# Kernel optimization log

Measured on AMD Instinct MI355X. Metric: run time of the kernel, lower is better.

Reference implementation:

```python
import jax, jax.numpy as jnp
import numpy as np
import math

B, T, C = 8, 2048, 1024
KEY_SIZE, VALUE_SIZE = 1024, 1024


def setup_inputs() -> dict:
    key = jax.random.key(0)
    ks = jax.random.split(key, 7)
    s = 1.0 / math.sqrt(C)
    return {
        "input": jax.random.normal(ks[0], (B, T, C), dtype=jnp.float32),
        "mask": jnp.ones((B, T, 1), dtype=jnp.float32),
        "Wq": jax.random.uniform(ks[1], (C, KEY_SIZE), jnp.float32, -s, s),
        "bq": jax.random.uniform(ks[2], (KEY_SIZE,), jnp.float32, -s, s),
        "Wk": jax.random.uniform(ks[3], (C, KEY_SIZE), jnp.float32, -s, s),
        "bk": jax.random.uniform(ks[4], (KEY_SIZE,), jnp.float32, -s, s),
        "Wv": jax.random.uniform(ks[5], (C, VALUE_SIZE), jnp.float32, -s, s),
        "bv": jax.random.uniform(ks[6], (VALUE_SIZE,), jnp.float32, -s, s),
    }


def reference(input, mask, Wq, bq, Wk, bk, Wv, bv):
    # QKV projections: [B, T, C] @ [C, K] -> [B, T, K]
    query = input @ Wq + bq
    keys = input @ Wk + bk
    values = input @ Wv + bv
    # scores[b, tq, tk] = query[b, tq, :] . keys[b, tk, :]
    scores = jnp.einsum("bqk,btk->bqt", query, keys) / math.sqrt(KEY_SIZE)
    # NOTE: softmax over the QUERY dimension (axis=1), as in the original (dim=1)
    attn = jax.nn.softmax(scores, axis=1)
    out = jnp.einsum("bqt,btv->bqv", attn, values)
    return out * mask
```

## Files before the change

kernel.cpp:

```cpp
#include <hip/hip_runtime.h>
#include <hip/hip_bf16.h>
#include <cstdint>

typedef __attribute__((ext_vector_type(8))) __bf16 bf16x8;
typedef __attribute__((ext_vector_type(4))) float f32x4;
typedef __attribute__((ext_vector_type(8))) unsigned short u16x8;

static __device__ __forceinline__ unsigned short f2b(float f) {
    union { float f; unsigned u; } v; v.f = f;
    unsigned r = v.u + 0x7fffu + ((v.u >> 16) & 1u);
    return (unsigned short)(r >> 16);
}
static __device__ __forceinline__ float b2f(unsigned short b) {
    union { unsigned u; float f; } v; v.u = ((unsigned)b) << 16;
    return v.f;
}

#define LL16(g, l) __builtin_amdgcn_global_load_lds( \
    (const __attribute__((address_space(1))) void*)(g), \
    (__attribute__((address_space(3))) void*)(l), 16, 0, 0)

#define BAR() __builtin_amdgcn_s_barrier()
#define WAIT_VM6() asm volatile("s_waitcnt vmcnt(6)" ::: "memory")
#define WAIT_VM0() asm volatile("s_waitcnt vmcnt(0)" ::: "memory")

__global__ void conv_f32_bf16(const float* __restrict__ in,
                              unsigned short* __restrict__ out, long n8) {
    long i = (long)blockIdx.x * blockDim.x + threadIdx.x;
    if (i >= n8) return;
    const float4* p = (const float4*)in + i * 2;
    float4 a = p[0], b = p[1];
    u16x8 r;
    r[0] = f2b(a.x); r[1] = f2b(a.y); r[2] = f2b(a.z); r[3] = f2b(a.w);
    r[4] = f2b(b.x); r[5] = f2b(b.y); r[6] = f2b(b.z); r[7] = f2b(b.w);
    *(u16x8*)(out + i * 8) = r;
}

__global__ void transpose_w(const float* __restrict__ w0,
                            const float* __restrict__ w1,
                            const float* __restrict__ w2,
                            unsigned short* __restrict__ out) {
    __shared__ float tile[32][33];
    int z = blockIdx.z;
    const float* W = (z == 0) ? w0 : (z == 1) ? w1 : w2;
    int n0 = blockIdx.x * 32, c0 = blockIdx.y * 32;
    int tx = threadIdx.x & 31, ty = threadIdx.x >> 5;
    #pragma unroll
    for (int i = 0; i < 32; i += 8)
        tile[ty + i][tx] = W[(long)(c0 + ty + i) * 1024 + n0 + tx];
    __syncthreads();
    unsigned short* o = out + (long)z * 1024 * 1024;
    #pragma unroll
    for (int i = 0; i < 32; i += 8)
        o[(long)(n0 + ty + i) * 1024 + c0 + tx] = f2b(tile[tx][ty + i]);
}

__global__ void scale_vt(unsigned short* __restrict__ Vt,
                         const float* __restrict__ colsum) {
    long i8 = ((long)blockIdx.x * 256 + threadIdx.x) * 8;
    int b = (int)(i8 >> 21);
    int rem = (int)(i8 & ((1 << 21) - 1));
    int t = rem & 2047;
    const float* cs = colsum + b * 2048 + t;
    u16x8 v = *(const u16x8*)(Vt + i8);
    u16x8 o;
    #pragma unroll
    for (int j = 0; j < 8; ++j) o[j] = f2b(b2f(v[j]) / cs[j]);
    *(u16x8*)(Vt + i8) = o;
}


#define RD_A(h) do { _Pragma("unroll") for (int mi = 2*(h); mi < 2*(h)+2; ++mi) { \
    af[mi][0] = *(const bf16x8*)(lds + aBase + baA + mi*1024 + cx0); \
    af[mi][1] = *(const bf16x8*)(lds + aBase + baA + mi*1024 + cx1); } } while (0)
#define RD_B(h) do { _Pragma("unroll") for (int nj = 2*(h); nj < 2*(h)+2; ++nj) { \
    bf[nj][0] = *(const bf16x8*)(lds + bBase + baB + nj*1024 + cx0); \
    bf[nj][1] = *(const bf16x8*)(lds + bBase + baB + nj*1024 + cx1); } } while (0)
#define MMA_Q(a, b) do { \
    __builtin_amdgcn_s_setprio(1); \
    _Pragma("unroll") for (int mi = 2*(a); mi < 2*(a)+2; ++mi) \
    _Pragma("unroll") for (int nj = 2*(b); nj < 2*(b)+2; ++nj) { \
        acc[mi][nj] = __builtin_amdgcn_mfma_f32_16x16x32_bf16( \
            af[mi][0], bf[nj][0], acc[mi][nj], 0, 0, 0); \
        acc[mi][nj] = __builtin_amdgcn_mfma_f32_16x16x32_bf16( \
            af[mi][1], bf[nj][1], acc[mi][nj], 0, 0, 0); } \
    __builtin_amdgcn_s_setprio(0); } while (0)

template<int MODE>
__global__ __launch_bounds__(512, 2)
void gemm256x128(const unsigned short* __restrict__ Aall,
                 const unsigned short* __restrict__ Ball,
                 void* __restrict__ Cv,
                 int M, int N, int K, int ldc,
                 long aStride, long bStride, long cStride,
                 const float* __restrict__ aux, float* __restrict__ colsum) {
    __shared__ unsigned short lds[73728];

    const int gx = gridDim.x, gy = gridDim.y;
    const int nxy = gx * gy;
    const int nwg = nxy * gridDim.z;
    const int orig = (blockIdx.z * gy + blockIdx.y) * gx + blockIdx.x;
    const int swz = (orig & 7) * (nwg >> 3) + (orig >> 3);
    const int bz = swz / nxy;
    const int rem = swz - bz * nxy;
    const int by = rem / gx;
    const int bx = rem - by * gx;

    const unsigned short* A  = Aall + (long)bz * aStride;
    const unsigned short* Bt = Ball + (long)bz * bStride;

    const int tid = threadIdx.x;
    const int lane = tid & 63;
    const int w = tid >> 6;
    const int wrow = w >> 1, wcol = w & 1;
    const int lr = lane & 15, lg = lane >> 4;

    const int bm = by * 256, bn = bx * 128;
    const int NT = K >> 6;

    const int r0 = tid >> 3;
    const int c0 = (tid & 7) ^ (r0 & 7);
    const unsigned short* sA0 = A  + (long)(bm + r0)       * K + c0 * 8;
    const unsigned short* sA1 = A  + (long)(bm + 64 + r0)  * K + c0 * 8;
    const unsigned short* sA2 = A  + (long)(bm + 128 + r0) * K + c0 * 8;
    const unsigned short* sA3 = A  + (long)(bm + 192 + r0) * K + c0 * 8;
    const unsigned short* sB0 = Bt + (long)(bn + r0)       * K + c0 * 8;
    const unsigned short* sB1 = Bt + (long)(bn + 64 + r0)  * K + c0 * 8;
    const int dstT = tid * 8;

    const int cx0 = (lg ^ (lr & 7)) * 8;
    const int cx1 = ((4 + lg) ^ (lr & 7)) * 8;
    const int baA = (wrow * 64 + lr) * 64;
    const int baB = (wcol * 64 + lr) * 64;

    bf16x8 af[4][2], bf[4][2];
    f32x4 acc[4][4] = {};

    #define STAGE(kt, ai, bi) do { const long ko = (long)(kt) * 64; \
        LL16(sA0 + ko, lds + (ai) * 16384 + dstT); \
        LL16(sA1 + ko, lds + (ai) * 16384 + 4096 + dstT); \
        LL16(sA2 + ko, lds + (ai) * 16384 + 8192 + dstT); \
        LL16(sA3 + ko, lds + (ai) * 16384 + 12288 + dstT); \
        LL16(sB0 + ko, lds + 49152 + (bi) * 8192 + dstT); \
        LL16(sB1 + ko, lds + 49152 + (bi) * 8192 + 4096 + dstT); } while (0)

    STAGE(0, 0, 0);
    STAGE(1, 1, 1);

    int bCur = 0, bNxt = 1, bStg = 2;
    for (int t = 0; t < NT; ++t) {
        if (t == NT - 1) { WAIT_VM0(); } else { WAIT_VM6(); }
        BAR();
        if (t + 2 < NT) STAGE(t + 2, bStg, bStg);

        const int aBase = bCur * 16384;
        const int bBase = 49152 + bCur * 8192;
        RD_A(0); RD_B(0);
        MMA_Q(0, 0);
        RD_A(1);
        MMA_Q(1, 0);
        RD_B(1);
        MMA_Q(1, 1);
        MMA_Q(0, 1);

        const int tmp = bCur; bCur = bNxt; bNxt = bStg; bStg = tmp;
    }
    BAR();

    if (MODE != 3) {
        unsigned short* C = (unsigned short*)Cv + (long)bz * cStride;
        float* cs = colsum + (long)bz * 2048;
        #pragma unroll
        for (int nj = 0; nj < 4; ++nj) {
            const int cl = wcol * 64 + nj * 16 + lr;
            const int cb = cl >> 3, cIn = cl & 7;
            float colB = (MODE == 0) ? aux[bn + cl] : 0.f;
            float psum = 0.f;
            #pragma unroll
            for (int mi = 0; mi < 4; ++mi) {
                #pragma unroll
                for (int r = 0; r < 4; ++r) {
                    const int rl = wrow * 64 + mi * 16 + lg * 4 + r;
                    float v = acc[mi][nj][r];
                    if (MODE == 0) v += colB;
                    else if (MODE == 1) v += aux[bm + rl];
                    else { v = __expf(v * 0.03125f); psum += v; }
                    lds[rl * 128 + ((cb ^ ((rl & 7) << 1)) << 3) + cIn] = f2b(v);
                }
            }
            if (MODE == 2) {
                psum += __shfl_xor(psum, 16);
                psum += __shfl_xor(psum, 32);
                if (lg == 0) atomicAdd(&cs[bn + cl], psum);
            }
        }
        BAR();
        #pragma unroll
        for (int it = 0; it < 8; ++it) {
            int lin = it * 512 + tid;
            int row = lin >> 4;
            int c = lin & 15;
            u16x8 v = *(const u16x8*)&lds[row * 128 + ((c ^ ((row & 7) << 1)) << 3)];
            *(u16x8*)&C[(long)(bm + row) * ldc + bn + c * 8] = v;
        }
    } else {
        float* C = (float*)Cv + (long)bz * cStride;
        const float* mk = aux + (long)bz * 2048;
        float* ft = (float*)lds;
        #pragma unroll
        for (int h = 0; h < 2; ++h) {
            if (h) BAR();
            if ((wrow >> 1) == h) {
                #pragma unroll
                for (int nj = 0; nj < 4; ++nj) {
                    const int cl = wcol * 64 + nj * 16 + lr;
                    const int cf = cl >> 2, cIn = cl & 3;
                    #pragma unroll
                    for (int mi = 0; mi < 4; ++mi) {
                        #pragma unroll
                        for (int r = 0; r < 4; ++r) {
                            const int rl2 = (wrow & 1) * 64 + mi * 16 + lg * 4 + r;
                            const int gr = bm + h * 128 + rl2;
                            ft[rl2 * 128 + ((cf ^ ((rl2 & 7) << 2)) << 2) + cIn] =
                                acc[mi][nj][r] * mk[gr];
                        }
                    }
                }
            }
            BAR();
            #pragma unroll
            for (int it = 0; it < 8; ++it) {
                int lin = it * 512 + tid;
                int row = lin >> 5;
                int cf = lin & 31;
                float4 v = *(const float4*)&ft[row * 128 + ((cf ^ ((row & 7) << 2)) << 2)];
                *(float4*)&C[(long)(bm + h * 128 + row) * ldc + bn + cf * 4] = v;
            }
        }
    }
    #undef STAGE
}

extern "C" void kernel_launch(void* const* d_in, const int* in_sizes, int n_in,
                              void* d_out, int out_size, void* d_ws, size_t ws_size,
                              hipStream_t stream) {
    const float* x    = (const float*)d_in[0];
    const float* mask = (const float*)d_in[1];
    const float* Wq   = (const float*)d_in[2];
    const float* bq   = (const float*)d_in[3];
    const float* Wk   = (const float*)d_in[4];
    const float* bk   = (const float*)d_in[5];
    const float* Wv   = (const float*)d_in[6];
    const float* bv   = (const float*)d_in[7];
    float* out = (float*)d_out;

    const long MT = 16384;
    unsigned short* Xb = (unsigned short*)d_ws;
    unsigned short* Wt = Xb + MT * 1024;
    unsigned short* Q  = Wt + 3L * 1024 * 1024;
    unsigned short* Kk = Q  + MT * 1024;
    unsigned short* Vt = Kk + MT * 1024;
    unsigned short* E  = Vt + 8L * 1024 * 2048;
    float* colsum = (float*)(E + 8L * 2048 * 2048);
    size_t need = (size_t)((char*)(colsum + 8 * 2048) - (char*)d_ws);
    if (ws_size < need) return;

    conv_f32_bf16<<<(MT * 1024) / 8 / 256, 256, 0, stream>>>(x, Xb, (MT * 1024) / 8);
    transpose_w<<<dim3(32, 32, 3), 256, 0, stream>>>(Wq, Wk, Wv, Wt);
    gemm256x128<0><<<dim3(8, 64, 1), 512, 0, stream>>>(
        Xb, Wt, Q, 16384, 1024, 1024, 1024, 0, 0, 0, bq, nullptr);
    gemm256x128<0><<<dim3(8, 64, 1), 512, 0, stream>>>(
        Xb, Wt + 1048576, Kk, 16384, 1024, 1024, 1024, 0, 0, 0, bk, nullptr);
    gemm256x128<1><<<dim3(16, 4, 8), 512, 0, stream>>>(
        Wt + 2097152, Xb, Vt, 1024, 2048, 1024, 2048,
        0, 2048L * 1024, 1024L * 2048, bv, nullptr);
    hipMemsetAsync(colsum, 0, 8 * 2048 * sizeof(float), stream);
    gemm256x128<2><<<dim3(16, 8, 8), 512, 0, stream>>>(
        Q, Kk, E, 2048, 2048, 1024, 2048,
        2048L * 1024, 2048L * 1024, 2048L * 2048, nullptr, colsum);
    scale_vt<<<8192, 256, 0, stream>>>(Vt, colsum);
    gemm256x128<3><<<dim3(8, 8, 8), 512, 0, stream>>>(
        E, Vt, out, 2048, 1024, 2048, 1024,
        2048L * 2048, 1024L * 2048, 2048L * 1024, mask, nullptr);
}
```

Before: 334.0 us.

## Shrink GEMM tile to 128x128 with 4 waves and double-buffered LDS

Replaces the 256x128 tile, 8-wave, triple-buffered GEMM with a 128x128 tile, 4-wave kernel that double-buffers LDS. Each iteration loads all fragments and then runs all MFMAs, with a trailing barrier before the next stage is issued. Block mapping is remapped into groups of 4 columns for L2 locality, and every launch grid is doubled. Lower LDS use should allow more resident blocks, at the cost of more global traffic per flop and an extra barrier per k-step.

```diff
diff --git a/kernel.cpp b/kernel.cpp
--- a/kernel.cpp
+++ b/kernel.cpp
@@ -21,7 +21,7 @@
     (__attribute__((address_space(3))) void*)(l), 16, 0, 0)
 
 #define BAR() __builtin_amdgcn_s_barrier()
-#define WAIT_VM6() asm volatile("s_waitcnt vmcnt(6)" ::: "memory")
+#define WAIT_VM8() asm volatile("s_waitcnt vmcnt(8)" ::: "memory")
 #define WAIT_VM0() asm volatile("s_waitcnt vmcnt(0)" ::: "memory")
 
 __global__ void conv_f32_bf16(const float* __restrict__ in,
@@ -70,31 +70,15 @@
 }
 
 
-#define RD_A(h) do { _Pragma("unroll") for (int mi = 2*(h); mi < 2*(h)+2; ++mi) { \
-    af[mi][0] = *(const bf16x8*)(lds + aBase + baA + mi*1024 + cx0); \
-    af[mi][1] = *(const bf16x8*)(lds + aBase + baA + mi*1024 + cx1); } } while (0)
-#define RD_B(h) do { _Pragma("unroll") for (int nj = 2*(h); nj < 2*(h)+2; ++nj) { \
-    bf[nj][0] = *(const bf16x8*)(lds + bBase + baB + nj*1024 + cx0); \
-    bf[nj][1] = *(const bf16x8*)(lds + bBase + baB + nj*1024 + cx1); } } while (0)
-#define MMA_Q(a, b) do { \
-    __builtin_amdgcn_s_setprio(1); \
-    _Pragma("unroll") for (int mi = 2*(a); mi < 2*(a)+2; ++mi) \
-    _Pragma("unroll") for (int nj = 2*(b); nj < 2*(b)+2; ++nj) { \
-        acc[mi][nj] = __builtin_amdgcn_mfma_f32_16x16x32_bf16( \
-            af[mi][0], bf[nj][0], acc[mi][nj], 0, 0, 0); \
-        acc[mi][nj] = __builtin_amdgcn_mfma_f32_16x16x32_bf16( \
-            af[mi][1], bf[nj][1], acc[mi][nj], 0, 0, 0); } \
-    __builtin_amdgcn_s_setprio(0); } while (0)
-
 template<int MODE>
-__global__ __launch_bounds__(512, 2)
-void gemm256x128(const unsigned short* __restrict__ Aall,
-                 const unsigned short* __restrict__ Ball,
-                 void* __restrict__ Cv,
-                 int M, int N, int K, int ldc,
-                 long aStride, long bStride, long cStride,
-                 const float* __restrict__ aux, float* __restrict__ colsum) {
-    __shared__ unsigned short lds[73728];
+__global__ __launch_bounds__(256, 2)
+void gemm128(const unsigned short* __restrict__ Aall,
+             const unsigned short* __restrict__ Ball,
+             void* __restrict__ Cv,
+             int M, int N, int K, int ldc,
+             long aStride, long bStride, long cStride,
+             const float* __restrict__ aux, float* __restrict__ colsum) {
+    __shared__ unsigned short lds[32768];
 
     const int gx = gridDim.x, gy = gridDim.y;
     const int nxy = gx * gy;
@@ -103,8 +87,10 @@
     const int swz = (orig & 7) * (nwg >> 3) + (orig >> 3);
     const int bz = swz / nxy;
     const int rem = swz - bz * nxy;
-    const int by = rem / gx;
-    const int bx = rem - by * gx;
+    const int sb = rem / (gy * 4);
+    const int r2 = rem - sb * (gy * 4);
+    const int by = r2 >> 2;
+    const int bx = sb * 4 + (r2 & 3);
 
     const unsigned short* A  = Aall + (long)bz * aStride;
     const unsigned short* Bt = Ball + (long)bz * bStride;
@@ -115,17 +101,19 @@
     const int wrow = w >> 1, wcol = w & 1;
     const int lr = lane & 15, lg = lane >> 4;
 
-    const int bm = by * 256, bn = bx * 128;
+    const int bm = by * 128, bn = bx * 128;
     const int NT = K >> 6;
 
     const int r0 = tid >> 3;
     const int c0 = (tid & 7) ^ (r0 & 7);
-    const unsigned short* sA0 = A  + (long)(bm + r0)       * K + c0 * 8;
-    const unsigned short* sA1 = A  + (long)(bm + 64 + r0)  * K + c0 * 8;
-    const unsigned short* sA2 = A  + (long)(bm + 128 + r0) * K + c0 * 8;
-    const unsigned short* sA3 = A  + (long)(bm + 192 + r0) * K + c0 * 8;
-    const unsigned short* sB0 = Bt + (long)(bn + r0)       * K + c0 * 8;
-    const unsigned short* sB1 = Bt + (long)(bn + 64 + r0)  * K + c0 * 8;
+    const unsigned short* sA0 = A  + (long)(bm + r0)      * K + c0 * 8;
+    const unsigned short* sA1 = A  + (long)(bm + 32 + r0) * K + c0 * 8;
+    const unsigned short* sA2 = A  + (long)(bm + 64 + r0) * K + c0 * 8;
+    const unsigned short* sA3 = A  + (long)(bm + 96 + r0) * K + c0 * 8;
+    const unsigned short* sB0 = Bt + (long)(bn + r0)      * K + c0 * 8;
+    const unsigned short* sB1 = Bt + (long)(bn + 32 + r0) * K + c0 * 8;
+    const unsigned short* sB2 = Bt + (long)(bn + 64 + r0) * K + c0 * 8;
+    const unsigned short* sB3 = Bt + (long)(bn + 96 + r0) * K + c0 * 8;
     const int dstT = tid * 8;
 
     const int cx0 = (lg ^ (lr & 7)) * 8;
@@ -136,36 +124,51 @@
     bf16x8 af[4][2], bf[4][2];
     f32x4 acc[4][4] = {};
 
-    #define STAGE(kt, ai, bi) do { const long ko = (long)(kt) * 64; \
-        LL16(sA0 + ko, lds + (ai) * 16384 + dstT); \
-        LL16(sA1 + ko, lds + (ai) * 16384 + 4096 + dstT); \
-        LL16(sA2 + ko, lds + (ai) * 16384 + 8192 + dstT); \
-        LL16(sA3 + ko, lds + (ai) * 16384 + 12288 + dstT); \
-        LL16(sB0 + ko, lds + 49152 + (bi) * 8192 + dstT); \
-        LL16(sB1 + ko, lds + 49152 + (bi) * 8192 + 4096 + dstT); } while (0)
-
-    STAGE(0, 0, 0);
-    STAGE(1, 1, 1);
-
-    int bCur = 0, bNxt = 1, bStg = 2;
+    #define STAGE(kt, buf) do { const long ko = (long)(kt) * 64; \
+        LL16(sA0 + ko, lds + (buf) * 8192 + dstT); \
+        LL16(sA1 + ko, lds + (buf) * 8192 + 2048 + dstT); \
+        LL16(sA2 + ko, lds + (buf) * 8192 + 4096 + dstT); \
+        LL16(sA3 + ko, lds + (buf) * 8192 + 6144 + dstT); \
+        LL16(sB0 + ko, lds + 16384 + (buf) * 8192 + dstT); \
+        LL16(sB1 + ko, lds + 16384 + (buf) * 8192 + 2048 + dstT); \
+        LL16(sB2 + ko, lds + 16384 + (buf) * 8192 + 4096 + dstT); \
+        LL16(sB3 + ko, lds + 16384 + (buf) * 8192 + 6144 + dstT); } while (0)
+
+    STAGE(0, 0);
+    STAGE(1, 1);
+
     for (int t = 0; t < NT; ++t) {
-        if (t == NT - 1) { WAIT_VM0(); } else { WAIT_VM6(); }
-        BAR();
-        if (t + 2 < NT) STAGE(t + 2, bStg, bStg);
-
-        const int aBase = bCur * 16384;
-        const int bBase = 49152 + bCur * 8192;
-        RD_A(0); RD_B(0);
-        MMA_Q(0, 0);
-        RD_A(1);
-        MMA_Q(1, 0);
-        RD_B(1);
-        MMA_Q(1, 1);
-        MMA_Q(0, 1);
-
-        const int tmp = bCur; bCur = bNxt; bNxt = bStg; bStg = tmp;
+        if (t < NT - 1) { WAIT_VM8(); } else { WAIT_VM0(); }
+        BAR();
+
+        const int aB = (t & 1) * 8192;
+        const int bB = 16384 + (t & 1) * 8192;
+        #pragma unroll
+        for (int mi = 0; mi < 4; ++mi) {
+            af[mi][0] = *(const bf16x8*)(lds + aB + baA + mi * 1024 + cx0);
+            af[mi][1] = *(const bf16x8*)(lds + aB + baA + mi * 1024 + cx1);
+        }
+        #pragma unroll
+        for (int nj = 0; nj < 4; ++nj) {
+            bf[nj][0] = *(const bf16x8*)(lds + bB + baB + nj * 1024 + cx0);
+            bf[nj][1] = *(const bf16x8*)(lds + bB + baB + nj * 1024 + cx1);
+        }
+        __builtin_amdgcn_s_setprio(1);
+        #pragma unroll
+        for (int mi = 0; mi < 4; ++mi)
+            #pragma unroll
+            for (int nj = 0; nj < 4; ++nj) {
+                acc[mi][nj] = __builtin_amdgcn_mfma_f32_16x16x32_bf16(
+                    af[mi][0], bf[nj][0], acc[mi][nj], 0, 0, 0);
+                acc[mi][nj] = __builtin_amdgcn_mfma_f32_16x16x32_bf16(
+                    af[mi][1], bf[nj][1], acc[mi][nj], 0, 0, 0);
+            }
+        __builtin_amdgcn_s_setprio(0);
+
+        BAR();
+        if (t + 2 < NT) STAGE(t + 2, t & 1);
     }
-    BAR();
+    #undef STAGE
 
     if (MODE != 3) {
         unsigned short* C = (unsigned short*)Cv + (long)bz * cStride;
@@ -197,7 +200,7 @@
         BAR();
         #pragma unroll
         for (int it = 0; it < 8; ++it) {
-            int lin = it * 512 + tid;
+            int lin = it * 256 + tid;
             int row = lin >> 4;
             int c = lin & 15;
             u16x8 v = *(const u16x8*)&lds[row * 128 + ((c ^ ((row & 7) << 1)) << 3)];
@@ -208,37 +211,29 @@
         const float* mk = aux + (long)bz * 2048;
         float* ft = (float*)lds;
         #pragma unroll
-        for (int h = 0; h < 2; ++h) {
-            if (h) BAR();
-            if ((wrow >> 1) == h) {
+        for (int nj = 0; nj < 4; ++nj) {
+            const int cl = wcol * 64 + nj * 16 + lr;
+            const int cf = cl >> 2, cIn = cl & 3;
+            #pragma unroll
+            for (int mi = 0; mi < 4; ++mi) {
                 #pragma unroll
-                for (int nj = 0; nj < 4; ++nj) {
-                    const int cl = wcol * 64 + nj * 16 + lr;
-                    const int cf = cl >> 2, cIn = cl & 3;
-                    #pragma unroll
-                    for (int mi = 0; mi < 4; ++mi) {
-                        #pragma unroll
-                        for (int r = 0; r < 4; ++r) {
-                            const int rl2 = (wrow & 1) * 64 + mi * 16 + lg * 4 + r;
-                            const int gr = bm + h * 128 + rl2;
-                            ft[rl2 * 128 + ((cf ^ ((rl2 & 7) << 2)) << 2) + cIn] =
-                                acc[mi][nj][r] * mk[gr];
-                        }
-                    }
+                for (int r = 0; r < 4; ++r) {
+                    const int rl = wrow * 64 + mi * 16 + lg * 4 + r;
+                    ft[rl * 128 + ((cf ^ ((rl & 7) << 2)) << 2) + cIn] =
+                        acc[mi][nj][r] * mk[bm + rl];
                 }
             }
-            BAR();
-            #pragma unroll
-            for (int it = 0; it < 8; ++it) {
-                int lin = it * 512 + tid;
-                int row = lin >> 5;
-                int cf = lin & 31;
-                float4 v = *(const float4*)&ft[row * 128 + ((cf ^ ((row & 7) << 2)) << 2)];
-                *(float4*)&C[(long)(bm + h * 128 + row) * ldc + bn + cf * 4] = v;
-            }
+        }
+        BAR();
+        #pragma unroll
+        for (int it = 0; it < 16; ++it) {
+            int lin = it * 256 + tid;
+            int row = lin >> 5;
+            int cf = lin & 31;
+            float4 v = *(const float4*)&ft[row * 128 + ((cf ^ ((row & 7) << 2)) << 2)];
+            *(float4*)&C[(long)(bm + row) * ldc + bn + cf * 4] = v;
         }
     }
-    #undef STAGE
 }
 
 extern "C" void kernel_launch(void* const* d_in, const int* in_sizes, int n_in,
@@ -267,19 +262,19 @@
 
     conv_f32_bf16<<<(MT * 1024) / 8 / 256, 256, 0, stream>>>(x, Xb, (MT * 1024) / 8);
     transpose_w<<<dim3(32, 32, 3), 256, 0, stream>>>(Wq, Wk, Wv, Wt);
-    gemm256x128<0><<<dim3(8, 64, 1), 512, 0, stream>>>(
+    gemm128<0><<<dim3(8, 128, 1), 256, 0, stream>>>(
         Xb, Wt, Q, 16384, 1024, 1024, 1024, 0, 0, 0, bq, nullptr);
-    gemm256x128<0><<<dim3(8, 64, 1), 512, 0, stream>>>(
+    gemm128<0><<<dim3(8, 128, 1), 256, 0, stream>>>(
         Xb, Wt + 1048576, Kk, 16384, 1024, 1024, 1024, 0, 0, 0, bk, nullptr);
-    gemm256x128<1><<<dim3(16, 4, 8), 512, 0, stream>>>(
+    gemm128<1><<<dim3(16, 8, 8), 256, 0, stream>>>(
         Wt + 2097152, Xb, Vt, 1024, 2048, 1024, 2048,
         0, 2048L * 1024, 1024L * 2048, bv, nullptr);
     hipMemsetAsync(colsum, 0, 8 * 2048 * sizeof(float), stream);
-    gemm256x128<2><<<dim3(16, 8, 8), 512, 0, stream>>>(
+    gemm128<2><<<dim3(16, 16, 8), 256, 0, stream>>>(
         Q, Kk, E, 2048, 2048, 1024, 2048,
         2048L * 1024, 2048L * 1024, 2048L * 2048, nullptr, colsum);
     scale_vt<<<8192, 256, 0, stream>>>(Vt, colsum);
-    gemm256x128<3><<<dim3(8, 8, 8), 512, 0, stream>>>(
+    gemm128<3><<<dim3(8, 16, 8), 256, 0, stream>>>(
         E, Vt, out, 2048, 1024, 2048, 1024,
         2048L * 2048, 1024L * 2048, 2048L * 1024, mask, nullptr);
 }
```

Measured after the change: 311.8 us. 1.07x faster.
